# Performance work log

Measured on AMD Instinct MI355X. Metric: run time of the kernel, lower is better.

## Reference

```python
import jax, jax.numpy as jnp
import numpy as np

DEPTH = 9            # perfect binary tree depth (root=level 0, leaves=level DEPTH)
N_TREES = 128
H = 256              # h_size == x_size (ndata['h'] init uses x_size)
NPT = 2 ** (DEPTH + 1) - 1   # 1023 nodes per tree
N = N_TREES * NPT            # 130944 total nodes


def _levels():
    """Static per-level (node, left-child, right-child) global index arrays."""
    base = np.arange(N_TREES, dtype=np.int64)[:, None] * NPT
    out = []
    for l in range(DEPTH + 1):
        loc = np.arange(2 ** l - 1, 2 ** (l + 1) - 1, dtype=np.int64)
        nodes = (base + loc[None, :]).reshape(-1)
        if l < DEPTH:
            cl = (base + (2 * loc + 1)[None, :]).reshape(-1)
            cr = (base + (2 * loc + 2)[None, :]).reshape(-1)
        else:
            cl = cr = None
        out.append((jnp.asarray(nodes),
                    None if cl is None else jnp.asarray(cl),
                    None if cr is None else jnp.asarray(cr)))
    return out


def setup_inputs() -> dict:
    key = jax.random.key(0)
    ks = jax.random.split(key, 10)
    s = lambda d: 1.0 / np.sqrt(d)
    return {
        "wordid": jax.random.randint(ks[0], (N,), 0, 32000),
        "mask":   jax.random.randint(ks[1], (N,), 0, 2),
        "emb":    jax.random.normal(ks[2], (32000, H), jnp.float32) * 0.02,
        "W_iou":  jax.random.normal(ks[3], (H, 3 * H), jnp.float32) * s(H),
        "U_iou":  jax.random.normal(ks[4], (2 * H, 3 * H), jnp.float32) * s(2 * H),
        "U_f_w":  jax.random.normal(ks[5], (2 * H, 2 * H), jnp.float32) * s(2 * H),
        "U_f_b":  jax.random.normal(ks[6], (2 * H,), jnp.float32) * 0.01,
        "b_iou":  jax.random.normal(ks[7], (3 * H,), jnp.float32) * 0.01,
        "lin_w":  jax.random.normal(ks[8], (H, 4), jnp.float32) * s(H),
        "lin_b":  jax.random.normal(ks[9], (4,), jnp.float32) * 0.01,
    }


def _apply_node(iou, b_iou, c_in, mh_in):
    i, o, u = jnp.split(iou + b_iou, 3, axis=1)
    i, o, u = jax.nn.sigmoid(i), jax.nn.sigmoid(o), jnp.tanh(u)
    c = i * u + c_in
    h = o * jnp.tanh(c)
    return h, c, jnp.maximum(h, mh_in)


def reference(wordid, mask, emb, W_iou, U_iou, U_f_w, U_f_b, b_iou, lin_w, lin_b):
    levels = _levels()
    x = emb[wordid * mask]                                  # [N, H]
    iou0 = (x @ W_iou) * mask[:, None].astype(x.dtype)      # leaf/pre-set iou [N, 3H]

    h = jnp.zeros((N, H), x.dtype)
    c = jnp.zeros((N, H), x.dtype)
    mh = jnp.zeros((N, H), x.dtype)

    # leaves: no incoming messages -> apply with preset iou, c=0, max_h=0
    li, _, _ = levels[DEPTH]
    hh, cc, mm = _apply_node(iou0[li], b_iou, 0.0, 0.0)
    h, c, mh = h.at[li].set(hh), c.at[li].set(cc), mh.at[li].set(mm)

    # internal levels, bottom-up (DGL prop_nodes_topo)
    for l in range(DEPTH - 1, -1, -1):
        ni, cl, cr = levels[l]
        h_cat = jnp.concatenate([h[cl], h[cr]], axis=1)     # [M, 2H]
        f = jax.nn.sigmoid(h_cat @ U_f_w + U_f_b)           # [M, 2H]
        fl, fr = jnp.split(f, 2, axis=1)
        c_red = fl * c[cl] + fr * c[cr]
        mh_red = jnp.maximum(mh[cl], mh[cr])
        iou = h_cat @ U_iou                                  # overwrites preset iou
        hh, cc, mm = _apply_node(iou, b_iou, c_red, mh_red)
        h, c, mh = h.at[ni].set(hh), c.at[ni].set(cc), mh.at[ni].set(mm)

    return (h + mh) @ lin_w + lin_b                         # logits [N, num_classes]
```

## Files before the change

### kernel.cpp

```cpp
#include <hip/hip_runtime.h>
#include <hip/hip_bf16.h>


#define NTREES 128
#define NPT    1023
#define HS     256
#define NNODES (NTREES * NPT)
#define NL     (NTREES * 512)

typedef __hip_bfloat16 bf16;
typedef unsigned short us8 __attribute__((ext_vector_type(8)));
typedef unsigned short us4 __attribute__((ext_vector_type(4)));
typedef short bf16x8 __attribute__((ext_vector_type(8)));
typedef float f32x4 __attribute__((ext_vector_type(4)));

typedef __attribute__((address_space(1))) const void gvoid;
typedef __attribute__((address_space(3))) void svoid;
#define GLD16(gp, lp) \
    __builtin_amdgcn_global_load_lds((gvoid*)(gp), (svoid*)(lp), 16, 0, 0)

__device__ __forceinline__ float bits2f(unsigned short b) {
    return __uint_as_float(((unsigned)b) << 16);
}
__device__ __forceinline__ unsigned short f2bits(float x) {
    bf16 h = __float2bfloat16(x);
    return *reinterpret_cast<unsigned short*>(&h);
}
__device__ __forceinline__ float fsigm(float x) {
    return __builtin_amdgcn_rcpf(1.0f + __expf(-x));
}
__device__ __forceinline__ float ftanh(float x) {
    return 1.0f - 2.0f * __builtin_amdgcn_rcpf(1.0f + __expf(2.0f * x));
}

#define WT_ELEMS (768 * 256)
#define UT_ELEMS (1280 * 512)
#define PW_ELEMS (WT_ELEMS + UT_ELEMS)
#define PREPB    ((PW_ELEMS + 255) / 256)

__global__ __launch_bounds__(256) void prep_all(
    const float* __restrict__ W_iou, const float* __restrict__ U_f_w,
    const float* __restrict__ U_iou,
    const int* __restrict__ wordid, const int* __restrict__ mask,
    const float* __restrict__ emb,
    bf16* __restrict__ Wt, bf16* __restrict__ Ut, bf16* __restrict__ x_bf)
{
    if (blockIdx.x < PREPB) {
        const int i = blockIdx.x * 256 + threadIdx.x;
        if (i < WT_ELEMS) {
            const int n = i >> 8, k = i & 255;
            Wt[i] = __float2bfloat16(W_iou[k * 768 + n]);
        } else if (i < PW_ELEMS) {
            const int j = i - WT_ELEMS;
            const int n = j >> 9, k = j & 511;
            const float v = (n < 512) ? U_f_w[k * 512 + n]
                                      : U_iou[k * 768 + (n - 512)];
            Ut[j] = __float2bfloat16(v);
        }
        return;
    }
    const int wave = threadIdx.x >> 6, lane = threadIdx.x & 63;
    const int gr   = (blockIdx.x - PREPB) * 4 + wave;
    const int node = (gr >> 9) * NPT + 511 + (gr & 511);
    const int j0   = lane * 4;
    us4 v;
    if (mask[node]) {
        const float4 f = *(const float4*)(emb + (long)wordid[node] * HS + j0);
        v[0] = f2bits(f.x); v[1] = f2bits(f.y);
        v[2] = f2bits(f.z); v[3] = f2bits(f.w);
    } else {
        v[0] = v[1] = v[2] = v[3] = 0;
    }
    *(us4*)(x_bf + (long)gr * HS + j0) = v;
}

__global__ __launch_bounds__(256) void leaf_fused(
    const bf16* __restrict__ x_bf, const bf16* __restrict__ Wt,
    const float* __restrict__ b_iou,
    bf16* __restrict__ h_s, bf16* __restrict__ cm_s,
    bf16* __restrict__ s_full, const int tree0)
{
    __shared__ __align__(16) short a_s[2][128 * 32];
    __shared__ __align__(16) short b_s[2][96 * 32];
    const int t    = threadIdx.x;
    const int bm0  = blockIdx.x * 128;
    const int c0   = blockIdx.y * 32;
    const int lane = t & 63, wave = t >> 6;
    const int l4a = lane >> 2, k8 = (lane & 3) * 8;

    const bf16* aSrc[2];
    #pragma unroll
    for (int q = 0; q < 2; ++q) {
        const int row = (wave * 2 + q) * 16 + l4a;
        aSrc[q] = x_bf + (long)(tree0 * 512 + bm0 + row) * HS + k8;
    }
    const int bCnt = (wave < 3) ? 2 : 0;
    const int bStart = wave * 2;
    const bf16* bSrc[2];
    #pragma unroll
    for (int q = 0; q < 2; ++q) {
        int rb = (bStart + q) * 16 + l4a;
        if (rb > 95) rb = 95;
        const int g = rb >> 5, jl = rb & 31;
        bSrc[q] = Wt + (long)(g * 256 + c0 + jl) * 256 + k8;
    }

    const int wr = wave >> 1, wc = wave & 1;
    const int fr = lane & 15, l4 = lane >> 4;

    f32x4 acc[4][3];
    #pragma unroll
    for (int i = 0; i < 4; ++i)
        #pragma unroll
        for (int g = 0; g < 3; ++g) acc[i][g] = (f32x4){0.f, 0.f, 0.f, 0.f};

    auto stage = [&](int buf, int kt) {
        #pragma unroll
        for (int q = 0; q < 2; ++q)
            GLD16(aSrc[q] + kt, &a_s[buf][(wave * 2 + q) * 512]);
        #pragma unroll
        for (int q = 0; q < 2; ++q)
            if (q < bCnt) GLD16(bSrc[q] + kt, &b_s[buf][(bStart + q) * 512]);
    };

    stage(0, 0);
    __syncthreads();
    int cur = 0;
    for (int kt = 0; kt < 256; kt += 32) {
        const int nk = kt + 32;
        if (nk < 256) stage(cur ^ 1, nk);
        bf16x8 af[4], bg[3];
        #pragma unroll
        for (int i = 0; i < 4; ++i)
            af[i] = *(const bf16x8*)&a_s[cur][(wr * 64 + i * 16 + fr) * 32 + l4 * 8];
        #pragma unroll
        for (int g = 0; g < 3; ++g)
            bg[g] = *(const bf16x8*)&b_s[cur][(g * 32 + wc * 16 + fr) * 32 + l4 * 8];
        #pragma unroll
        for (int i = 0; i < 4; ++i)
            #pragma unroll
            for (int g = 0; g < 3; ++g)
                acc[i][g] = __builtin_amdgcn_mfma_f32_16x16x32_bf16(
                    bg[g], af[i], acc[i][g], 0, 0, 0);
        __syncthreads();
        cur ^= 1;
    }

    const int j0 = c0 + wc * 16 + l4 * 4;
    const float4 bi4 = *(const float4*)(b_iou + j0);
    const float4 bo4 = *(const float4*)(b_iou + 256 + j0);
    const float4 bu4 = *(const float4*)(b_iou + 512 + j0);
    #pragma unroll
    for (int i = 0; i < 4; ++i) {
        const int r    = bm0 + wr * 64 + i * 16 + fr;
        const int gr   = tree0 * 512 + r;
        const int node = (gr >> 9) * NPT + 511 + (gr & 511);
        us4 sh, ss; us8 scm;
        #pragma unroll
        for (int q = 0; q < 4; ++q) {
            const float iv = fsigm(acc[i][0][q] + ((const float*)&bi4)[q]);
            const float ov = fsigm(acc[i][1][q] + ((const float*)&bo4)[q]);
            const float uv = ftanh(acc[i][2][q] + ((const float*)&bu4)[q]);
            const float cv  = iv * uv;
            const float hv  = ov * ftanh(cv);
            const float mhv = fmaxf(hv, 0.0f);
            sh[q] = f2bits(hv); ss[q] = f2bits(hv + mhv);
            scm[2 * q] = f2bits(cv); scm[2 * q + 1] = f2bits(mhv);
        }
        *(us4*)(h_s + (long)r * HS + j0)        = sh;
        *(us8*)(cm_s + (long)r * 512 + j0 * 2)  = scm;
        *(us4*)(s_full + (long)node * HS + j0)  = ss;
    }
}

__global__ __launch_bounds__(256) void level_fused(
    const bf16* __restrict__ h_child, const bf16* __restrict__ cm_c,
    const bf16* __restrict__ Ut,
    const float* __restrict__ U_f_b, const float* __restrict__ b_iou,
    bf16* __restrict__ h_p, bf16* __restrict__ cm_p,
    bf16* __restrict__ s_full, const int lvl, const int M, const int tree0)
{
    __shared__ __align__(16) short a_s[2][128 * 32];
    __shared__ __align__(16) short b_s[2][160 * 32];
    const int t    = threadIdx.x;
    const int bm0  = blockIdx.x * 128;
    const int c0   = blockIdx.y * 32;
    const int lane = t & 63, wave = t >> 6;
    const int l4a = lane >> 2, k8 = (lane & 3) * 8;

    const bf16* aSrc[2];
    #pragma unroll
    for (int q = 0; q < 2; ++q) {
        int p = bm0 + (wave * 2 + q) * 16 + l4a;
        if (p >= M) p = M - 1;
        const int tl  = p >> lvl;
        const int idx = p & ((1 << lvl) - 1);
        const int cls = tl * (2 << lvl) + 2 * idx;
        aSrc[q] = h_child + (long)cls * HS + k8;
    }
    const int bCnt   = (wave < 2) ? 3 : 2;
    const int bStart = (wave < 2) ? wave * 3 : 6 + (wave - 2) * 2;
    const bf16* bSrc[3];
    #pragma unroll
    for (int q = 0; q < 3; ++q) {
        int rb = (bStart + q) * 16 + l4a;
        if (rb > 159) rb = 159;
        const int g = rb >> 5, jl = rb & 31;
        bSrc[q] = Ut + (long)(g * 256 + c0 + jl) * 512 + k8;
    }

    const int wr = wave >> 1, wc = wave & 1;
    const int fr = lane & 15, l4 = lane >> 4;

    f32x4 acc[4][5];
    #pragma unroll
    for (int i = 0; i < 4; ++i)
        #pragma unroll
        for (int g = 0; g < 5; ++g) acc[i][g] = (f32x4){0.f, 0.f, 0.f, 0.f};

    auto stage = [&](int buf, int kt) {
        #pragma unroll
        for (int q = 0; q < 2; ++q)
            GLD16(aSrc[q] + kt, &a_s[buf][(wave * 2 + q) * 512]);
        #pragma unroll
        for (int q = 0; q < 3; ++q)
            if (q < bCnt) GLD16(bSrc[q] + kt, &b_s[buf][(bStart + q) * 512]);
    };

    stage(0, 0);
    __syncthreads();
    int cur = 0;
    for (int kt = 0; kt < 512; kt += 32) {
        const int nk = kt + 32;
        if (nk < 512) stage(cur ^ 1, nk);
        bf16x8 af[4], bg[5];
        #pragma unroll
        for (int i = 0; i < 4; ++i)
            af[i] = *(const bf16x8*)&a_s[cur][(wr * 64 + i * 16 + fr) * 32 + l4 * 8];
        #pragma unroll
        for (int g = 0; g < 5; ++g)
            bg[g] = *(const bf16x8*)&b_s[cur][(g * 32 + wc * 16 + fr) * 32 + l4 * 8];
        #pragma unroll
        for (int i = 0; i < 4; ++i)
            #pragma unroll
            for (int g = 0; g < 5; ++g)
                acc[i][g] = __builtin_amdgcn_mfma_f32_16x16x32_bf16(
                    bg[g], af[i], acc[i][g], 0, 0, 0);
        __syncthreads();
        cur ^= 1;
    }

    const int j0 = c0 + wc * 16 + l4 * 4;
    const float4 bfl4 = *(const float4*)(U_f_b + j0);
    const float4 bfr4 = *(const float4*)(U_f_b + 256 + j0);
    const float4 bi4  = *(const float4*)(b_iou + j0);
    const float4 bo4  = *(const float4*)(b_iou + 256 + j0);
    const float4 bu4  = *(const float4*)(b_iou + 512 + j0);
    #pragma unroll
    for (int i = 0; i < 4; ++i) {
        const int r  = bm0 + wr * 64 + i * 16 + fr;
        const int rc = r < M ? r : M - 1;
        const int tl   = rc >> lvl;
        const int idx  = rc & ((1 << lvl) - 1);
        const int cls  = tl * (2 << lvl) + 2 * idx;
        const int node = (tree0 + tl) * NPT + (1 << lvl) - 1 + idx;
        const us8 cml = *(const us8*)(cm_c + (long)cls * 512 + j0 * 2);
        const us8 cmr = *(const us8*)(cm_c + (long)(cls + 1) * 512 + j0 * 2);
        us4 sh, ss; us8 scm;
        #pragma unroll
        for (int q = 0; q < 4; ++q) {
            const float flv = fsigm(acc[i][0][q] + ((const float*)&bfl4)[q]);
            const float frv = fsigm(acc[i][1][q] + ((const float*)&bfr4)[q]);
            const float iv  = fsigm(acc[i][2][q] + ((const float*)&bi4)[q]);
            const float ov  = fsigm(acc[i][3][q] + ((const float*)&bo4)[q]);
            const float uv  = ftanh(acc[i][4][q] + ((const float*)&bu4)[q]);
            const float ccl = bits2f(cml[2 * q]), mhl = bits2f(cml[2 * q + 1]);
            const float ccr = bits2f(cmr[2 * q]), mhr = bits2f(cmr[2 * q + 1]);
            const float cv  = iv * uv + flv * ccl + frv * ccr;
            const float hv  = ov * ftanh(cv);
            const float mhv = fmaxf(hv, fmaxf(mhl, mhr));
            sh[q] = f2bits(hv); ss[q] = f2bits(hv + mhv);
            scm[2 * q] = f2bits(cv); scm[2 * q + 1] = f2bits(mhv);
        }
        if (r < M) {
            *(us4*)(h_p + (long)r * HS + j0)       = sh;
            *(us8*)(cm_p + (long)r * 512 + j0 * 2) = scm;
            *(us4*)(s_full + (long)node * HS + j0) = ss;
        }
    }
}

__global__ __launch_bounds__(256) void logits_k(
    const bf16* __restrict__ s_full, const float* __restrict__ lin_w,
    const float* __restrict__ lin_b, float* __restrict__ out)
{
    const int wave = threadIdx.x >> 6, lane = threadIdx.x & 63;
    const int node = blockIdx.x * 4 + wave;
    const int j0   = lane * 4;
    const us4 v = *(const us4*)(s_full + (long)node * HS + j0);
    float p0 = 0.f, p1 = 0.f, p2 = 0.f, p3 = 0.f;
    #pragma unroll
    for (int q = 0; q < 4; ++q) {
        const float s  = bits2f(v[q]);
        const float4 w = *(const float4*)(lin_w + (j0 + q) * 4);
        p0 += s * w.x; p1 += s * w.y; p2 += s * w.z; p3 += s * w.w;
    }
    #pragma unroll
    for (int m = 1; m < 64; m <<= 1) {
        p0 += __shfl_xor(p0, m); p1 += __shfl_xor(p1, m);
        p2 += __shfl_xor(p2, m); p3 += __shfl_xor(p3, m);
    }
    if (lane == 0) {
        float4 r;
        r.x = p0 + lin_b[0]; r.y = p1 + lin_b[1];
        r.z = p2 + lin_b[2]; r.w = p3 + lin_b[3];
        *(float4*)(out + (long)node * 4) = r;
    }
}

extern "C" void kernel_launch(void* const* d_in, const int* in_sizes, int n_in,
                              void* d_out, int out_size, void* d_ws, size_t ws_size,
                              hipStream_t stream) {
    const int*   wordid = (const int*)d_in[0];
    const int*   mask   = (const int*)d_in[1];
    const float* emb    = (const float*)d_in[2];
    const float* W_iou  = (const float*)d_in[3];
    const float* U_iou  = (const float*)d_in[4];
    const float* U_f_w  = (const float*)d_in[5];
    const float* U_f_b  = (const float*)d_in[6];
    const float* b_iou  = (const float*)d_in[7];
    const float* lin_w  = (const float*)d_in[8];
    const float* lin_b  = (const float*)d_in[9];
    float* out = (float*)d_out;

    const size_t wElems = (size_t)PW_ELEMS;
    const size_t sElems = (size_t)NNODES * HS;
    const size_t xElems = (size_t)NL * HS;
    auto need = [&](int T) -> size_t {
        return (wElems + sElems + xElems + (size_t)T * 589824) * 2;
    };
    int T = 8;
    const int cands[4] = {128, 64, 32, 16};
    for (int ci = 0; ci < 4; ++ci) {
        if (need(cands[ci]) <= ws_size) { T = cands[ci]; break; }
    }

    bf16* Wt     = (bf16*)d_ws;
    bf16* Ut     = Wt + WT_ELEMS;
    bf16* s_full = Ut + UT_ELEMS;
    bf16* x_bf   = s_full + sElems;
    bf16* hA  = x_bf + xElems;
    bf16* cmA = hA  + (size_t)T * 512 * HS;
    bf16* hB  = cmA + (size_t)T * 512 * HS * 2;
    bf16* cmB = hB  + (size_t)T * 256 * HS;

    prep_all<<<PREPB + NL / 4, 256, 0, stream>>>(
        W_iou, U_f_w, U_iou, wordid, mask, emb, Wt, Ut, x_bf);

    for (int tree0 = 0; tree0 < NTREES; tree0 += T) {
        leaf_fused<<<dim3(T * 512 / 128, 8), 256, 0, stream>>>(
            x_bf, Wt, b_iou, hA, cmA, s_full, tree0);
        bool childIsA = true;
        for (int l = 8; l >= 0; --l) {
            bf16 *hc, *cmc, *hp, *cmp;
            if (childIsA) { hc = hA; cmc = cmA; hp = hB; cmp = cmB; }
            else          { hc = hB; cmc = cmB; hp = hA; cmp = cmA; }
            const int M = T << l;
            level_fused<<<dim3((M + 127) / 128, 8), 256, 0, stream>>>(
                hc, cmc, Ut, U_f_b, b_iou, hp, cmp, s_full, l, M, tree0);
            childIsA = !childIsA;
        }
    }
    logits_k<<<NNODES / 4, 256, 0, stream>>>(s_full, lin_w, lin_b, out);
}
```

Measured before the change: 422.8 us.

## Fuse output projection into level kernels via atomics and enlarge row tiles

Removes the bf16 s_full buffer of (h+max_h) per node and the separate logits pass. Each level kernel now projects its own output slice onto lin_w and accumulates partial logits into a zeroed fp32 buffer with atomicAdd. A small final kernel adds the bias. Blocks also grow from 128 to 256 rows with 512 threads, which halves the B-tile loading per row but cuts the grid size for the small upper levels and adds atomic traffic.

```diff
diff --git a/kernel.cpp b/kernel.cpp
--- a/kernel.cpp
+++ b/kernel.cpp
@@ -37,13 +37,16 @@
 #define UT_ELEMS (1280 * 512)
 #define PW_ELEMS (WT_ELEMS + UT_ELEMS)
 #define PREPB    ((PW_ELEMS + 255) / 256)
+#define GATB     (NL / 4)
+#define ZB       ((NNODES + 255) / 256)
 
 __global__ __launch_bounds__(256) void prep_all(
     const float* __restrict__ W_iou, const float* __restrict__ U_f_w,
     const float* __restrict__ U_iou,
     const int* __restrict__ wordid, const int* __restrict__ mask,
     const float* __restrict__ emb,
-    bf16* __restrict__ Wt, bf16* __restrict__ Ut, bf16* __restrict__ x_bf)
+    bf16* __restrict__ Wt, bf16* __restrict__ Ut, bf16* __restrict__ x_bf,
+    float* __restrict__ pl)
 {
     if (blockIdx.x < PREPB) {
         const int i = blockIdx.x * 256 + threadIdx.x;
@@ -59,31 +62,36 @@
         }
         return;
     }
-    const int wave = threadIdx.x >> 6, lane = threadIdx.x & 63;
-    const int gr   = (blockIdx.x - PREPB) * 4 + wave;
-    const int node = (gr >> 9) * NPT + 511 + (gr & 511);
-    const int j0   = lane * 4;
-    us4 v;
-    if (mask[node]) {
-        const float4 f = *(const float4*)(emb + (long)wordid[node] * HS + j0);
-        v[0] = f2bits(f.x); v[1] = f2bits(f.y);
-        v[2] = f2bits(f.z); v[3] = f2bits(f.w);
-    } else {
-        v[0] = v[1] = v[2] = v[3] = 0;
-    }
-    *(us4*)(x_bf + (long)gr * HS + j0) = v;
-}
-
-__global__ __launch_bounds__(256) void leaf_fused(
+    if (blockIdx.x < PREPB + GATB) {
+        const int wave = threadIdx.x >> 6, lane = threadIdx.x & 63;
+        const int gr   = (blockIdx.x - PREPB) * 4 + wave;
+        const int node = (gr >> 9) * NPT + 511 + (gr & 511);
+        const int j0   = lane * 4;
+        us4 v;
+        if (mask[node]) {
+            const float4 f = *(const float4*)(emb + (long)wordid[node] * HS + j0);
+            v[0] = f2bits(f.x); v[1] = f2bits(f.y);
+            v[2] = f2bits(f.z); v[3] = f2bits(f.w);
+        } else {
+            v[0] = v[1] = v[2] = v[3] = 0;
+        }
+        *(us4*)(x_bf + (long)gr * HS + j0) = v;
+        return;
+    }
+    const int i = (blockIdx.x - PREPB - GATB) * 256 + threadIdx.x;
+    if (i < NNODES) *(f32x4*)(pl + (long)i * 4) = (f32x4){0.f, 0.f, 0.f, 0.f};
+}
+
+__global__ __launch_bounds__(512) void leaf_fused(
     const bf16* __restrict__ x_bf, const bf16* __restrict__ Wt,
-    const float* __restrict__ b_iou,
+    const float* __restrict__ b_iou, const float* __restrict__ lin_w,
     bf16* __restrict__ h_s, bf16* __restrict__ cm_s,
-    bf16* __restrict__ s_full, const int tree0)
+    float* __restrict__ pl, const int tree0)
 {
-    __shared__ __align__(16) short a_s[2][128 * 32];
+    __shared__ __align__(16) short a_s[2][256 * 32];
     __shared__ __align__(16) short b_s[2][96 * 32];
     const int t    = threadIdx.x;
-    const int bm0  = blockIdx.x * 128;
+    const int bm0  = blockIdx.x * 256;
     const int c0   = blockIdx.y * 32;
     const int lane = t & 63, wave = t >> 6;
     const int l4a = lane >> 2, k8 = (lane & 3) * 8;
@@ -94,15 +102,13 @@
         const int row = (wave * 2 + q) * 16 + l4a;
         aSrc[q] = x_bf + (long)(tree0 * 512 + bm0 + row) * HS + k8;
     }
-    const int bCnt = (wave < 3) ? 2 : 0;
-    const int bStart = wave * 2;
-    const bf16* bSrc[2];
-    #pragma unroll
-    for (int q = 0; q < 2; ++q) {
-        int rb = (bStart + q) * 16 + l4a;
+    const int bCnt = (wave < 6) ? 1 : 0;
+    const bf16* bSrc0;
+    {
+        int rb = wave * 16 + l4a;
         if (rb > 95) rb = 95;
         const int g = rb >> 5, jl = rb & 31;
-        bSrc[q] = Wt + (long)(g * 256 + c0 + jl) * 256 + k8;
+        bSrc0 = Wt + (long)(g * 256 + c0 + jl) * 256 + k8;
     }
 
     const int wr = wave >> 1, wc = wave & 1;
@@ -118,9 +124,7 @@
         #pragma unroll
         for (int q = 0; q < 2; ++q)
             GLD16(aSrc[q] + kt, &a_s[buf][(wave * 2 + q) * 512]);
-        #pragma unroll
-        for (int q = 0; q < 2; ++q)
-            if (q < bCnt) GLD16(bSrc[q] + kt, &b_s[buf][(bStart + q) * 512]);
+        if (bCnt) GLD16(bSrc0 + kt, &b_s[buf][wave * 512]);
     };
 
     stage(0, 0);
@@ -155,7 +159,8 @@
         const int r    = bm0 + wr * 64 + i * 16 + fr;
         const int gr   = tree0 * 512 + r;
         const int node = (gr >> 9) * NPT + 511 + (gr & 511);
-        us4 sh, ss; us8 scm;
+        us4 sh; us8 scm;
+        float p0 = 0.f, p1 = 0.f, p2 = 0.f, p3 = 0.f;
         #pragma unroll
         for (int q = 0; q < 4; ++q) {
             const float iv = fsigm(acc[i][0][q] + ((const float*)&bi4)[q]);
@@ -164,26 +169,38 @@
             const float cv  = iv * uv;
             const float hv  = ov * ftanh(cv);
             const float mhv = fmaxf(hv, 0.0f);
-            sh[q] = f2bits(hv); ss[q] = f2bits(hv + mhv);
+            sh[q] = f2bits(hv);
             scm[2 * q] = f2bits(cv); scm[2 * q + 1] = f2bits(mhv);
+            const float s  = hv + mhv;
+            const float4 w = *(const float4*)(lin_w + (j0 + q) * 4);
+            p0 += s * w.x; p1 += s * w.y; p2 += s * w.z; p3 += s * w.w;
         }
         *(us4*)(h_s + (long)r * HS + j0)        = sh;
         *(us8*)(cm_s + (long)r * 512 + j0 * 2)  = scm;
-        *(us4*)(s_full + (long)node * HS + j0)  = ss;
-    }
-}
-
-__global__ __launch_bounds__(256) void level_fused(
+        p0 += __shfl_xor(p0, 16); p0 += __shfl_xor(p0, 32);
+        p1 += __shfl_xor(p1, 16); p1 += __shfl_xor(p1, 32);
+        p2 += __shfl_xor(p2, 16); p2 += __shfl_xor(p2, 32);
+        p3 += __shfl_xor(p3, 16); p3 += __shfl_xor(p3, 32);
+        if (l4 == 0) {
+            float* o = pl + (long)node * 4;
+            atomicAdd(o + 0, p0); atomicAdd(o + 1, p1);
+            atomicAdd(o + 2, p2); atomicAdd(o + 3, p3);
+        }
+    }
+}
+
+__global__ __launch_bounds__(512) void level_fused(
     const bf16* __restrict__ h_child, const bf16* __restrict__ cm_c,
     const bf16* __restrict__ Ut,
     const float* __restrict__ U_f_b, const float* __restrict__ b_iou,
+    const float* __restrict__ lin_w,
     bf16* __restrict__ h_p, bf16* __restrict__ cm_p,
-    bf16* __restrict__ s_full, const int lvl, const int M, const int tree0)
+    float* __restrict__ pl, const int lvl, const int M, const int tree0)
 {
-    __shared__ __align__(16) short a_s[2][128 * 32];
+    __shared__ __align__(16) short a_s[2][256 * 32];
     __shared__ __align__(16) short b_s[2][160 * 32];
     const int t    = threadIdx.x;
-    const int bm0  = blockIdx.x * 128;
+    const int bm0  = blockIdx.x * 256;
     const int c0   = blockIdx.y * 32;
     const int lane = t & 63, wave = t >> 6;
     const int l4a = lane >> 2, k8 = (lane & 3) * 8;
@@ -198,11 +215,11 @@
         const int cls = tl * (2 << lvl) + 2 * idx;
         aSrc[q] = h_child + (long)cls * HS + k8;
     }
-    const int bCnt   = (wave < 2) ? 3 : 2;
-    const int bStart = (wave < 2) ? wave * 3 : 6 + (wave - 2) * 2;
-    const bf16* bSrc[3];
-    #pragma unroll
-    for (int q = 0; q < 3; ++q) {
+    const int bCnt   = (wave < 2) ? 2 : 1;
+    const int bStart = (wave < 2) ? wave * 2 : wave + 2;
+    const bf16* bSrc[2];
+    #pragma unroll
+    for (int q = 0; q < 2; ++q) {
         int rb = (bStart + q) * 16 + l4a;
         if (rb > 159) rb = 159;
         const int g = rb >> 5, jl = rb & 31;
@@ -223,7 +240,7 @@
         for (int q = 0; q < 2; ++q)
             GLD16(aSrc[q] + kt, &a_s[buf][(wave * 2 + q) * 512]);
         #pragma unroll
-        for (int q = 0; q < 3; ++q)
+        for (int q = 0; q < 2; ++q)
             if (q < bCnt) GLD16(bSrc[q] + kt, &b_s[buf][(bStart + q) * 512]);
     };
 
@@ -266,7 +283,8 @@
         const int node = (tree0 + tl) * NPT + (1 << lvl) - 1 + idx;
         const us8 cml = *(const us8*)(cm_c + (long)cls * 512 + j0 * 2);
         const us8 cmr = *(const us8*)(cm_c + (long)(cls + 1) * 512 + j0 * 2);
-        us4 sh, ss; us8 scm;
+        us4 sh; us8 scm;
+        float p0 = 0.f, p1 = 0.f, p2 = 0.f, p3 = 0.f;
         #pragma unroll
         for (int q = 0; q < 4; ++q) {
             const float flv = fsigm(acc[i][0][q] + ((const float*)&bfl4)[q]);
@@ -279,42 +297,38 @@
             const float cv  = iv * uv + flv * ccl + frv * ccr;
             const float hv  = ov * ftanh(cv);
             const float mhv = fmaxf(hv, fmaxf(mhl, mhr));
-            sh[q] = f2bits(hv); ss[q] = f2bits(hv + mhv);
+            sh[q] = f2bits(hv);
             scm[2 * q] = f2bits(cv); scm[2 * q + 1] = f2bits(mhv);
-        }
+            const float s  = hv + mhv;
+            const float4 w = *(const float4*)(lin_w + (j0 + q) * 4);
+            p0 += s * w.x; p1 += s * w.y; p2 += s * w.z; p3 += s * w.w;
+        }
+        p0 += __shfl_xor(p0, 16); p0 += __shfl_xor(p0, 32);
+        p1 += __shfl_xor(p1, 16); p1 += __shfl_xor(p1, 32);
+        p2 += __shfl_xor(p2, 16); p2 += __shfl_xor(p2, 32);
+        p3 += __shfl_xor(p3, 16); p3 += __shfl_xor(p3, 32);
         if (r < M) {
             *(us4*)(h_p + (long)r * HS + j0)       = sh;
             *(us8*)(cm_p + (long)r * 512 + j0 * 2) = scm;
-            *(us4*)(s_full + (long)node * HS + j0) = ss;
-        }
-    }
-}
-
-__global__ __launch_bounds__(256) void logits_k(
-    const bf16* __restrict__ s_full, const float* __restrict__ lin_w,
-    const float* __restrict__ lin_b, float* __restrict__ out)
+            if (l4 == 0) {
+                float* o = pl + (long)node * 4;
+                atomicAdd(o + 0, p0); atomicAdd(o + 1, p1);
+                atomicAdd(o + 2, p2); atomicAdd(o + 3, p3);
+            }
+        }
+    }
+}
+
+__global__ __launch_bounds__(256) void out_final(
+    const float* __restrict__ pl, const float* __restrict__ lin_b,
+    float* __restrict__ out)
 {
-    const int wave = threadIdx.x >> 6, lane = threadIdx.x & 63;
-    const int node = blockIdx.x * 4 + wave;
-    const int j0   = lane * 4;
-    const us4 v = *(const us4*)(s_full + (long)node * HS + j0);
-    float p0 = 0.f, p1 = 0.f, p2 = 0.f, p3 = 0.f;
-    #pragma unroll
-    for (int q = 0; q < 4; ++q) {
-        const float s  = bits2f(v[q]);
-        const float4 w = *(const float4*)(lin_w + (j0 + q) * 4);
-        p0 += s * w.x; p1 += s * w.y; p2 += s * w.z; p3 += s * w.w;
-    }
-    #pragma unroll
-    for (int m = 1; m < 64; m <<= 1) {
-        p0 += __shfl_xor(p0, m); p1 += __shfl_xor(p1, m);
-        p2 += __shfl_xor(p2, m); p3 += __shfl_xor(p3, m);
-    }
-    if (lane == 0) {
-        float4 r;
-        r.x = p0 + lin_b[0]; r.y = p1 + lin_b[1];
-        r.z = p2 + lin_b[2]; r.w = p3 + lin_b[3];
-        *(float4*)(out + (long)node * 4) = r;
+    const int i = blockIdx.x * 256 + threadIdx.x;
+    if (i < NNODES) {
+        f32x4 v = *(const f32x4*)(pl + (long)i * 4);
+        v[0] += lin_b[0]; v[1] += lin_b[1];
+        v[2] += lin_b[2]; v[3] += lin_b[3];
+        *(f32x4*)(out + (long)i * 4) = v;
     }
 }
 
@@ -333,11 +347,11 @@
     const float* lin_b  = (const float*)d_in[9];
     float* out = (float*)d_out;
 
-    const size_t wElems = (size_t)PW_ELEMS;
-    const size_t sElems = (size_t)NNODES * HS;
-    const size_t xElems = (size_t)NL * HS;
+    const size_t wElems  = (size_t)PW_ELEMS;
+    const size_t xElems  = (size_t)NL * HS;
+    const size_t plBytes = (size_t)NNODES * 4 * 4;
     auto need = [&](int T) -> size_t {
-        return (wElems + sElems + xElems + (size_t)T * 589824) * 2;
+        return (wElems + xElems + (size_t)T * 589824) * 2 + plBytes;
     };
     int T = 8;
     const int cands[4] = {128, 64, 32, 16};
@@ -345,31 +359,31 @@
         if (need(cands[ci]) <= ws_size) { T = cands[ci]; break; }
     }
 
-    bf16* Wt     = (bf16*)d_ws;
-    bf16* Ut     = Wt + WT_ELEMS;
-    bf16* s_full = Ut + UT_ELEMS;
-    bf16* x_bf   = s_full + sElems;
-    bf16* hA  = x_bf + xElems;
-    bf16* cmA = hA  + (size_t)T * 512 * HS;
-    bf16* hB  = cmA + (size_t)T * 512 * HS * 2;
-    bf16* cmB = hB  + (size_t)T * 256 * HS;
-
-    prep_all<<<PREPB + NL / 4, 256, 0, stream>>>(
-        W_iou, U_f_w, U_iou, wordid, mask, emb, Wt, Ut, x_bf);
+    bf16* Wt   = (bf16*)d_ws;
+    bf16* Ut   = Wt + WT_ELEMS;
+    bf16* x_bf = Ut + UT_ELEMS;
+    float* pl  = (float*)(x_bf + xElems);
+    bf16* hA   = (bf16*)(pl + (size_t)NNODES * 4);
+    bf16* cmA  = hA  + (size_t)T * 512 * HS;
+    bf16* hB   = cmA + (size_t)T * 512 * HS * 2;
+    bf16* cmB  = hB  + (size_t)T * 256 * HS;
+
+    prep_all<<<PREPB + GATB + ZB, 256, 0, stream>>>(
+        W_iou, U_f_w, U_iou, wordid, mask, emb, Wt, Ut, x_bf, pl);
 
     for (int tree0 = 0; tree0 < NTREES; tree0 += T) {
-        leaf_fused<<<dim3(T * 512 / 128, 8), 256, 0, stream>>>(
-            x_bf, Wt, b_iou, hA, cmA, s_full, tree0);
+        leaf_fused<<<dim3(T * 512 / 256, 8), 512, 0, stream>>>(
+            x_bf, Wt, b_iou, lin_w, hA, cmA, pl, tree0);
         bool childIsA = true;
         for (int l = 8; l >= 0; --l) {
             bf16 *hc, *cmc, *hp, *cmp;
             if (childIsA) { hc = hA; cmc = cmA; hp = hB; cmp = cmB; }
             else          { hc = hB; cmc = cmB; hp = hA; cmp = cmA; }
             const int M = T << l;
-            level_fused<<<dim3((M + 127) / 128, 8), 256, 0, stream>>>(
-                hc, cmc, Ut, U_f_b, b_iou, hp, cmp, s_full, l, M, tree0);
+            level_fused<<<dim3((M + 255) / 256, 8), 512, 0, stream>>>(
+                hc, cmc, Ut, U_f_b, b_iou, lin_w, hp, cmp, pl, l, M, tree0);
             childIsA = !childIsA;
         }
     }
-    logits_k<<<NNODES / 4, 256, 0, stream>>>(s_full, lin_w, lin_b, out);
-}
+    out_final<<<(NNODES + 255) / 256, 256, 0, stream>>>(pl, lin_b, out);
+}
```

Measured after the change: 579.1 us. +37.0%, slower.
